# Performance work log

Hardware: AMD Instinct MI355X
Metric: run time of the kernel (lower is better)

The kernel has to match this reference:

```python
import jax, jax.numpy as jnp
import numpy as np

B, S, D = 8, 4096, 768
HEADS = 12
NEIGHBORS = 2
DILATION = 1
KERNEL = 1 + 2 * NEIGHBORS  # 5
DIM_HEAD = D // HEADS


def setup_inputs() -> dict:
    key = jax.random.key(0)
    ks = jax.random.split(key, 11)
    sc = 1.0 / np.sqrt(D)
    return {
        "x": jax.random.normal(ks[0], (B, S, D), dtype=jnp.float32),
        "Wq": jax.random.normal(ks[1], (D, D), dtype=jnp.float32) * sc,
        "bq": jax.random.normal(ks[2], (D,), dtype=jnp.float32) * 0.02,
        "Wk": jax.random.normal(ks[3], (D, D), dtype=jnp.float32) * sc,
        "bk": jax.random.normal(ks[4], (D,), dtype=jnp.float32) * 0.02,
        "Wv": jax.random.normal(ks[5], (D, D), dtype=jnp.float32) * sc,
        "bv": jax.random.normal(ks[6], (D,), dtype=jnp.float32) * 0.02,
        "Wo": jax.random.normal(ks[7], (D, D), dtype=jnp.float32) * sc,
        "bo": jax.random.normal(ks[8], (D,), dtype=jnp.float32) * 0.02,
        "gamma": jnp.ones((D,), dtype=jnp.float32),
        "beta": jnp.zeros((D,), dtype=jnp.float32),
    }


def _extract_seq_patches(x, kernel_size, dilation):
    # [B, S, D] -> [B, S, kernel_size, D] of dilated local windows, zero-padded.
    seq_len = x.shape[1]
    patch_size = kernel_size + (dilation - 1) * (kernel_size - 1)
    pad_r = (patch_size - 1) // 2
    pad_l = patch_size - pad_r - 1
    xp = jnp.pad(x, ((0, 0), (pad_l, pad_r), (0, 0)))
    # small fixed loop over kernel positions (kernel_size = 5)
    return jnp.stack([xp[:, i:i + seq_len] for i in range(0, patch_size, dilation)], axis=2)


def reference(x, Wq, bq, Wk, bk, Wv, bv, Wo, bo, gamma, beta):
    patches = _extract_seq_patches(x, KERNEL, DILATION)  # [B, S, K, D]
    q = x @ Wq + bq                                       # [B, S, D]
    k = patches @ Wk + bk                                 # [B, S, K, D]
    v = patches @ Wv + bv                                 # [B, S, K, D]
    # split heads
    q = q.reshape(B, S, HEADS, DIM_HEAD)
    k = k.reshape(B, S, KERNEL, HEADS, DIM_HEAD)
    v = v.reshape(B, S, KERNEL, HEADS, DIM_HEAD)
    scale = jnp.sqrt(jnp.asarray(DIM_HEAD, dtype=q.dtype))
    scores = jnp.einsum('bshd,bskhd->bshk', q, k) / scale  # [B, S, H, K]
    p = jax.nn.softmax(scores, axis=-1)
    att = jnp.einsum('bshk,bskhd->bshd', p, v)             # [B, S, H, dh]
    att = att.reshape(B, S, D)
    att = att @ Wo + bo
    y = att + x
    # LayerNorm over last dim
    mu = jnp.mean(y, axis=-1, keepdims=True)
    var = jnp.var(y, axis=-1, keepdims=True)
    y = (y - mu) / jnp.sqrt(var + 1e-5) * gamma + beta
    return y
```

## Files before the change

### kernel.cpp

```cpp
#include <hip/hip_runtime.h>

#define B_  8
#define S_  4096
#define D_  768
#define H_  12
#define M_  (B_ * S_)
#define NQKV_ 2304
#define NTILES 12

typedef unsigned short u16;
typedef __attribute__((ext_vector_type(4))) float  f32x4;
typedef __attribute__((ext_vector_type(8))) __bf16 bf16x8;
typedef __attribute__((ext_vector_type(4))) u16    u16x4;

#define GAS __attribute__((address_space(1)))
#define LAS __attribute__((address_space(3)))

__device__ __forceinline__ u16 f2bf(float f) {
    unsigned u = __float_as_uint(f);
    u += 0x7FFF + ((u >> 16) & 1);
    return (u16)(u >> 16);
}
__device__ __forceinline__ float bf2f(u16 h) {
    return __uint_as_float(((unsigned)h) << 16);
}

__device__ __forceinline__ void gload_lds16(const void* g, void* l) {
    __builtin_amdgcn_global_load_lds((const GAS void*)g, (LAS void*)l, 16, 0, 0);
}

__device__ __forceinline__ int xcd_swz(int bid, int nwg) {
    return (bid & 7) * (nwg >> 3) + (bid >> 3);
}

__global__ __launch_bounds__(256) void castx_kernel(const float* __restrict__ x,
                                                    u16* __restrict__ xb) {
    const int i = blockIdx.x * 256 + threadIdx.x;
    const float4 v = ((const float4*)x)[i];
    u16x4 o;
    o.x = f2bf(v.x); o.y = f2bf(v.y); o.z = f2bf(v.z); o.w = f2bf(v.w);
    ((u16x4*)xb)[i] = o;
}

__global__ __launch_bounds__(256) void wtrans_kernel(const float* __restrict__ Wq,
                                                     const float* __restrict__ Wk,
                                                     const float* __restrict__ Wv,
                                                     const float* __restrict__ Wo,
                                                     u16* __restrict__ Wb) {
    const float* W = (blockIdx.z == 0) ? Wq : (blockIdx.z == 1) ? Wk
                   : (blockIdx.z == 2) ? Wv : Wo;
    u16* O = Wb + (size_t)blockIdx.z * D_ * D_;
    __shared__ float tile[32][33];
    const int tx = threadIdx.x & 31, ty = threadIdx.x >> 5;
    const int k0 = blockIdx.y * 32, n0 = blockIdx.x * 32;
#pragma unroll
    for (int j = 0; j < 4; j++)
        tile[ty + j * 8][tx] = W[(size_t)(k0 + ty + j * 8) * D_ + n0 + tx];
    __syncthreads();
#pragma unroll
    for (int j = 0; j < 4; j++)
        O[(size_t)(n0 + ty + j * 8) * D_ + k0 + tx] = f2bf(tile[tx][ty + j * 8]);
}


#define PHASE_END(N)                                         \
    __builtin_amdgcn_sched_barrier(0);                       \
    asm volatile("s_waitcnt vmcnt(" #N ")" ::: "memory");    \
    __builtin_amdgcn_s_barrier();                            \
    __builtin_amdgcn_sched_barrier(0)

#define MFMA_Q(AF, BF, MO, NO)                                               \
    _Pragma("unroll") for (int mi = 0; mi < 4; ++mi)                         \
        _Pragma("unroll") for (int ni = 0; ni < 2; ++ni)                     \
            _Pragma("unroll") for (int kh = 0; kh < 2; ++kh)                 \
                acc[mi + MO][ni + NO] =                                      \
                    __builtin_amdgcn_mfma_f32_16x16x32_bf16(                 \
                        AF[mi][kh], BF[ni][kh], acc[mi + MO][ni + NO], 0, 0, 0)

template <int MODE>
__global__ __launch_bounds__(512, 2) void gemm8_kernel(
    const u16* __restrict__ A, const u16* __restrict__ Wb,
    const float* __restrict__ b0, const float* __restrict__ b1,
    const float* __restrict__ b2,
    u16* __restrict__ outb, const u16* __restrict__ xres) {
    extern __shared__ char lds[];

    const int t = threadIdx.x;
    const int w = t >> 6, l = t & 63;
    const int wm = w >> 2, wn = w & 3;

    const int NTN = (MODE == 0) ? 9 : 3;
    const int work = xcd_swz(blockIdx.x, gridDim.x);
    const int mt = work / NTN, nt = work % NTN;
    const int m0 = mt * 256;
    const int n0 = nt * 256;
    const int widx = (MODE == 0) ? (n0 / D_) : 3;
    const int n0w = n0 - ((MODE == 0) ? widx * D_ : 0);

    const int srow   = t >> 3;
    const int schunk = (t & 7) ^ (srow & 7);
    const u16* Asrc = A + (size_t)(m0 + srow) * D_ + schunk * 8;
    const u16* Bsrc = Wb + (size_t)widx * (D_ * D_) + (size_t)(n0w + srow) * D_ + schunk * 8;

    auto STAGE_A = [&](int h, int tk, int db) {
        const u16* s = Asrc + (size_t)(h * 128) * D_ + tk * 64;
        char* d = lds + db * 65536 + h * 16384 + (w << 10);
        gload_lds16(s, d);
        gload_lds16(s + 64 * D_, d + 8192);
    };
    auto STAGE_B = [&](int h, int tk, int db) {
        const u16* s = Bsrc + (size_t)(h * 128) * D_ + tk * 64;
        char* d = lds + db * 65536 + 32768 + h * 16384 + (w << 10);
        gload_lds16(s, d);
        gload_lds16(s + 64 * D_, d + 8192);
    };

    const int ck0 = (((l >> 4) ^ (l & 7)) << 4);
    const int ck1 = ((((l >> 4) + 4) ^ (l & 7)) << 4);
    const int aRowB = (wm * 128 + (l & 15)) * 128;
    const int bRowB = 32768 + (wn * 64 + (l & 15)) * 128;
#define LDSREAD(off) (*(const bf16x8*)(lds + (off)))

    f32x4 acc[8][4];
#pragma unroll
    for (int i = 0; i < 8; i++)
#pragma unroll
        for (int j = 0; j < 4; j++) acc[i][j] = (f32x4){0.f, 0.f, 0.f, 0.f};

    bf16x8 Alo[4][2], Ahi[4][2], Ba[2][2], Bb[2][2];

    STAGE_A(0, 0, 0); STAGE_A(1, 0, 0); STAGE_B(0, 0, 0); STAGE_B(1, 0, 0);
    STAGE_B(1, 1, 1); STAGE_A(0, 1, 1); STAGE_A(1, 1, 1);
    __builtin_amdgcn_sched_barrier(0);
    asm volatile("s_waitcnt vmcnt(6)" ::: "memory");
    __builtin_amdgcn_s_barrier();
    __builtin_amdgcn_sched_barrier(0);
#pragma unroll
    for (int mi = 0; mi < 4; ++mi) {
        Alo[mi][0] = LDSREAD(aRowB + mi * 2048 + ck0);
        Alo[mi][1] = LDSREAD(aRowB + mi * 2048 + ck1);
    }
#pragma unroll
    for (int ni = 0; ni < 2; ++ni) {
        Ba[ni][0] = LDSREAD(bRowB + ni * 2048 + ck0);
        Ba[ni][1] = LDSREAD(bRowB + ni * 2048 + ck1);
    }

    for (int X = 0; X < NTILES; ++X) {
        const int bX = X & 1;
        const int L0off = bX << 16;
        const int L1off = (bX ^ 1) << 16;
        int t1 = X + 1; if (t1 >= NTILES) t1 -= NTILES;
        int t2 = X + 2; if (t2 >= NTILES) t2 -= NTILES;

#pragma unroll
        for (int ni = 0; ni < 2; ++ni) {
            Bb[ni][0] = LDSREAD(L0off + bRowB + (ni + 2) * 2048 + ck0);
            Bb[ni][1] = LDSREAD(L0off + bRowB + (ni + 2) * 2048 + ck1);
        }
#pragma unroll
        for (int mi = 0; mi < 4; ++mi) {
            Ahi[mi][0] = LDSREAD(L0off + aRowB + (mi + 4) * 2048 + ck0);
            Ahi[mi][1] = LDSREAD(L0off + aRowB + (mi + 4) * 2048 + ck1);
        }
        STAGE_B(0, t1, bX ^ 1);
        MFMA_Q(Alo, Ba, 0, 0);
        PHASE_END(8);

        STAGE_B(1, t2, bX);
        MFMA_Q(Alo, Bb, 0, 2);
        PHASE_END(4);

#pragma unroll
        for (int mi = 0; mi < 4; ++mi) {
            Alo[mi][0] = LDSREAD(L1off + aRowB + mi * 2048 + ck0);
            Alo[mi][1] = LDSREAD(L1off + aRowB + mi * 2048 + ck1);
        }
        STAGE_A(0, t2, bX);
        MFMA_Q(Ahi, Ba, 4, 0);
        PHASE_END(4);

#pragma unroll
        for (int ni = 0; ni < 2; ++ni) {
            Ba[ni][0] = LDSREAD(L1off + bRowB + ni * 2048 + ck0);
            Ba[ni][1] = LDSREAD(L1off + bRowB + ni * 2048 + ck1);
        }
        STAGE_A(1, t2, bX);
        MFMA_Q(Ahi, Bb, 4, 2);
        PHASE_END(8);
    }

    const int crow0 = m0 + wm * 128 + ((l >> 4) << 2);
    const int ccol0 = n0 + wn * 64 + (l & 15);
    if (MODE == 0) {
        const float* bias = (widx == 0) ? b0 : (widx == 1) ? b1 : b2;
        const int bcol0 = ccol0 - widx * D_;
#pragma unroll
        for (int mi = 0; mi < 8; ++mi)
#pragma unroll
            for (int ni = 0; ni < 4; ++ni) {
                const float bv = bias[bcol0 + ni * 16];
#pragma unroll
                for (int r = 0; r < 4; ++r)
                    outb[(size_t)(crow0 + mi * 16 + r) * NQKV_ + ccol0 + ni * 16] =
                        f2bf(acc[mi][ni][r] + bv);
            }
    } else {
#pragma unroll
        for (int mi = 0; mi < 8; ++mi)
#pragma unroll
            for (int ni = 0; ni < 4; ++ni) {
                const int col = ccol0 + ni * 16;
                const float bv = b0[col];
#pragma unroll
                for (int r = 0; r < 4; ++r) {
                    const size_t idx = (size_t)(crow0 + mi * 16 + r) * D_ + col;
                    outb[idx] = f2bf(acc[mi][ni][r] + bv + bf2f(xres[idx]));
                }
            }
    }
}

__global__ __launch_bounds__(256) void attn_kernel(const u16* __restrict__ QKV,
                                                   const float* __restrict__ bk,
                                                   const float* __restrict__ bv,
                                                   u16* __restrict__ att) {
    const int gw = xcd_swz(blockIdx.x, gridDim.x) * 4 + (threadIdx.x >> 6);
    const int l  = threadIdx.x & 63;
    const int hq = gw % 3;
    const int m  = gw / 3;
    const int s  = m & (S_ - 1);
    const int col = hq * 256 + l * 4;
    const u16* base = QKV + (size_t)m * NQKV_;

    const u16x4 qv = *(const u16x4*)(base + col);
    float qf[4];
#pragma unroll
    for (int j = 0; j < 4; j++) qf[j] = bf2f(qv[j]);

    float sc[5];
#pragma unroll
    for (int i = 0; i < 5; i++) {
        const int sp = s + i - 2;
        float p;
        if (sp >= 0 && sp < S_) {
            const u16x4 kv = *(const u16x4*)(base + (i - 2) * NQKV_ + D_ + col);
            p = qf[0] * bf2f(kv[0]) + qf[1] * bf2f(kv[1])
              + qf[2] * bf2f(kv[2]) + qf[3] * bf2f(kv[3]);
        } else {
            const float4 kb = *(const float4*)(bk + col);
            p = qf[0] * kb.x + qf[1] * kb.y + qf[2] * kb.z + qf[3] * kb.w;
        }
#pragma unroll
        for (int off = 1; off < 16; off <<= 1) p += __shfl_xor(p, off, 64);
        sc[i] = p * 0.125f;
    }
    float mx = sc[0];
#pragma unroll
    for (int i = 1; i < 5; i++) mx = fmaxf(mx, sc[i]);
    float e[5], sum = 0.f;
#pragma unroll
    for (int i = 0; i < 5; i++) { e[i] = __expf(sc[i] - mx); sum += e[i]; }
    const float inv = 1.f / sum;

    float o[4] = {0.f, 0.f, 0.f, 0.f};
#pragma unroll
    for (int i = 0; i < 5; i++) {
        const float wgt = e[i] * inv;
        const int sp = s + i - 2;
        if (sp >= 0 && sp < S_) {
            const u16x4 vv = *(const u16x4*)(base + (i - 2) * NQKV_ + 2 * D_ + col);
#pragma unroll
            for (int j = 0; j < 4; j++) o[j] += wgt * bf2f(vv[j]);
        } else {
            const float4 vb = *(const float4*)(bv + col);
            o[0] += wgt * vb.x; o[1] += wgt * vb.y;
            o[2] += wgt * vb.z; o[3] += wgt * vb.w;
        }
    }
    u16x4 ov;
#pragma unroll
    for (int j = 0; j < 4; j++) ov[j] = f2bf(o[j]);
    *(u16x4*)(att + (size_t)m * D_ + col) = ov;
}

__global__ __launch_bounds__(256) void ln_kernel(const u16* __restrict__ Yb,
                                                 const float* __restrict__ gamma,
                                                 const float* __restrict__ beta,
                                                 float* __restrict__ out) {
    const int row = blockIdx.x;
    const u16* r = Yb + (size_t)row * D_;
    const int t = threadIdx.x;
    const float v0 = bf2f(r[t]), v1 = bf2f(r[t + 256]), v2 = bf2f(r[t + 512]);
    float s  = v0 + v1 + v2;
    float s2 = v0 * v0 + v1 * v1 + v2 * v2;
#pragma unroll
    for (int off = 32; off > 0; off >>= 1) {
        s  += __shfl_xor(s,  off, 64);
        s2 += __shfl_xor(s2, off, 64);
    }
    __shared__ float red[8];
    const int w = t >> 6, l = t & 63;
    if (l == 0) { red[w] = s; red[4 + w] = s2; }
    __syncthreads();
    s  = red[0] + red[1] + red[2] + red[3];
    s2 = red[4] + red[5] + red[6] + red[7];
    const float mu  = s * (1.f / 768.f);
    const float var = s2 * (1.f / 768.f) - mu * mu;
    const float inv = rsqrtf(var + 1e-5f);
    float* o = out + (size_t)row * D_;
    o[t]       = (v0 - mu) * inv * gamma[t]       + beta[t];
    o[t + 256] = (v1 - mu) * inv * gamma[t + 256] + beta[t + 256];
    o[t + 512] = (v2 - mu) * inv * gamma[t + 512] + beta[t + 512];
}

extern "C" void kernel_launch(void* const* d_in, const int* in_sizes, int n_in,
                              void* d_out, int out_size, void* d_ws, size_t ws_size,
                              hipStream_t stream) {
    const float* x     = (const float*)d_in[0];
    const float* Wq    = (const float*)d_in[1];
    const float* bq    = (const float*)d_in[2];
    const float* Wk    = (const float*)d_in[3];
    const float* bk    = (const float*)d_in[4];
    const float* Wv    = (const float*)d_in[5];
    const float* bv    = (const float*)d_in[6];
    const float* Wo    = (const float*)d_in[7];
    const float* bo    = (const float*)d_in[8];
    const float* gamma = (const float*)d_in[9];
    const float* beta  = (const float*)d_in[10];

    char* ws = (char*)d_ws;
    u16*   Wb  = (u16*)ws;
    u16*   xb  = (u16*)(ws + 4718592);
    u16*   QKV = (u16*)(ws + 4718592 + 50331648);
    u16*   yb  = QKV;
    u16*   att = (u16*)d_out;

    (void)hipFuncSetAttribute(reinterpret_cast<const void*>(&gemm8_kernel<0>),
                              hipFuncAttributeMaxDynamicSharedMemorySize, 131072);
    (void)hipFuncSetAttribute(reinterpret_cast<const void*>(&gemm8_kernel<1>),
                              hipFuncAttributeMaxDynamicSharedMemorySize, 131072);

    castx_kernel<<<(M_ * D_) / (256 * 4), 256, 0, stream>>>(x, xb);
    wtrans_kernel<<<dim3(24, 24, 4), 256, 0, stream>>>(Wq, Wk, Wv, Wo, Wb);
    gemm8_kernel<0><<<(M_ / 256) * 9, 512, 131072, stream>>>(xb, Wb, bq, bk, bv,
                                                             QKV, nullptr);
    attn_kernel<<<(M_ * 3) / 4, 256, 0, stream>>>(QKV, bk, bv, att);
    gemm8_kernel<1><<<(M_ / 256) * 3, 512, 131072, stream>>>(att, Wb, bo, nullptr, nullptr,
                                                             yb, xb);
    ln_kernel<<<M_, 256, 0, stream>>>(yb, gamma, beta, (float*)d_out);
}
```

Before: 329.9 us.

## Fully unroll GEMM main loop, relax barrier waits, and raise MFMA priority

Fully unrolls the 12-iteration k-loop so buffer selection and wrapped tile indices become compile-time constants. LDS reads now use precomputed per-buffer base pointers with immediate offsets. Two of the four per-phase barriers drop their vmcnt wait, and the last iteration skips the now-unneeded LDS prefetch reads. MFMA blocks are wrapped in s_setprio to favour matrix issue across waves. The aim is to cut address arithmetic and stalls in the pipelined loop, at the cost of larger code size and tighter reliance on correct wait counts for the async global-to-LDS loads.

Measured after the change: 327.3 us. No clear change (-0.8%).

```diff
diff --git a/kernel.cpp b/kernel.cpp
--- a/kernel.cpp
+++ b/kernel.cpp
@@ -63,19 +63,28 @@
 }
 
 
-#define PHASE_END(N)                                         \
+#define BAR()                                                \
+    __builtin_amdgcn_sched_barrier(0);                       \
+    __builtin_amdgcn_s_barrier();                            \
+    __builtin_amdgcn_sched_barrier(0)
+
+#define VMBAR(N)                                             \
     __builtin_amdgcn_sched_barrier(0);                       \
     asm volatile("s_waitcnt vmcnt(" #N ")" ::: "memory");    \
     __builtin_amdgcn_s_barrier();                            \
     __builtin_amdgcn_sched_barrier(0)
 
 #define MFMA_Q(AF, BF, MO, NO)                                               \
+    __builtin_amdgcn_s_setprio(1);                                           \
     _Pragma("unroll") for (int mi = 0; mi < 4; ++mi)                         \
         _Pragma("unroll") for (int ni = 0; ni < 2; ++ni)                     \
             _Pragma("unroll") for (int kh = 0; kh < 2; ++kh)                 \
                 acc[mi + MO][ni + NO] =                                      \
                     __builtin_amdgcn_mfma_f32_16x16x32_bf16(                 \
-                        AF[mi][kh], BF[ni][kh], acc[mi + MO][ni + NO], 0, 0, 0)
+                        AF[mi][kh], BF[ni][kh], acc[mi + MO][ni + NO], 0, 0, 0); \
+    __builtin_amdgcn_s_setprio(0)
+
+#define RD(p, imm) (*(const bf16x8*)((p) + (imm)))
 
 template <int MODE>
 __global__ __launch_bounds__(512, 2) void gemm8_kernel(
@@ -119,7 +128,10 @@
     const int ck1 = ((((l >> 4) + 4) ^ (l & 7)) << 4);
     const int aRowB = (wm * 128 + (l & 15)) * 128;
     const int bRowB = 32768 + (wn * 64 + (l & 15)) * 128;
-#define LDSREAD(off) (*(const bf16x8*)(lds + (off)))
+    const char* aC0[2] = { lds + aRowB + ck0, lds + 65536 + aRowB + ck0 };
+    const char* aC1[2] = { lds + aRowB + ck1, lds + 65536 + aRowB + ck1 };
+    const char* bC0[2] = { lds + bRowB + ck0, lds + 65536 + bRowB + ck0 };
+    const char* bC1[2] = { lds + bRowB + ck1, lds + 65536 + bRowB + ck1 };
 
     f32x4 acc[8][4];
 #pragma unroll
@@ -137,57 +149,61 @@
     __builtin_amdgcn_sched_barrier(0);
 #pragma unroll
     for (int mi = 0; mi < 4; ++mi) {
-        Alo[mi][0] = LDSREAD(aRowB + mi * 2048 + ck0);
-        Alo[mi][1] = LDSREAD(aRowB + mi * 2048 + ck1);
+        Alo[mi][0] = RD(aC0[0], mi * 2048);
+        Alo[mi][1] = RD(aC1[0], mi * 2048);
     }
 #pragma unroll
     for (int ni = 0; ni < 2; ++ni) {
-        Ba[ni][0] = LDSREAD(bRowB + ni * 2048 + ck0);
-        Ba[ni][1] = LDSREAD(bRowB + ni * 2048 + ck1);
-    }
-
+        Ba[ni][0] = RD(bC0[0], ni * 2048);
+        Ba[ni][1] = RD(bC1[0], ni * 2048);
+    }
+
+#pragma unroll
     for (int X = 0; X < NTILES; ++X) {
-        const int bX = X & 1;
-        const int L0off = bX << 16;
-        const int L1off = (bX ^ 1) << 16;
-        int t1 = X + 1; if (t1 >= NTILES) t1 -= NTILES;
-        int t2 = X + 2; if (t2 >= NTILES) t2 -= NTILES;
+        const int c = X & 1;
+        const int o = c ^ 1;
+        const int t1 = (X + 1 < NTILES) ? X + 1 : X + 1 - NTILES;
+        const int t2 = (X + 2 < NTILES) ? X + 2 : X + 2 - NTILES;
 
 #pragma unroll
         for (int ni = 0; ni < 2; ++ni) {
-            Bb[ni][0] = LDSREAD(L0off + bRowB + (ni + 2) * 2048 + ck0);
-            Bb[ni][1] = LDSREAD(L0off + bRowB + (ni + 2) * 2048 + ck1);
+            Bb[ni][0] = RD(bC0[c], (ni + 2) * 2048);
+            Bb[ni][1] = RD(bC1[c], (ni + 2) * 2048);
         }
 #pragma unroll
         for (int mi = 0; mi < 4; ++mi) {
-            Ahi[mi][0] = LDSREAD(L0off + aRowB + (mi + 4) * 2048 + ck0);
-            Ahi[mi][1] = LDSREAD(L0off + aRowB + (mi + 4) * 2048 + ck1);
-        }
-        STAGE_B(0, t1, bX ^ 1);
+            Ahi[mi][0] = RD(aC0[c], (mi + 4) * 2048);
+            Ahi[mi][1] = RD(aC1[c], (mi + 4) * 2048);
+        }
+        STAGE_B(0, t1, o);
         MFMA_Q(Alo, Ba, 0, 0);
-        PHASE_END(8);
-
-        STAGE_B(1, t2, bX);
+        BAR();
+
+        STAGE_B(1, t2, c);
         MFMA_Q(Alo, Bb, 0, 2);
-        PHASE_END(4);
-
-#pragma unroll
-        for (int mi = 0; mi < 4; ++mi) {
-            Alo[mi][0] = LDSREAD(L1off + aRowB + mi * 2048 + ck0);
-            Alo[mi][1] = LDSREAD(L1off + aRowB + mi * 2048 + ck1);
-        }
-        STAGE_A(0, t2, bX);
+        VMBAR(4);
+
+        if (X + 1 < NTILES) {
+#pragma unroll
+            for (int mi = 0; mi < 4; ++mi) {
+                Alo[mi][0] = RD(aC0[o], mi * 2048);
+                Alo[mi][1] = RD(aC1[o], mi * 2048);
+            }
+        }
+        STAGE_A(0, t2, c);
         MFMA_Q(Ahi, Ba, 4, 0);
-        PHASE_END(4);
-
-#pragma unroll
-        for (int ni = 0; ni < 2; ++ni) {
-            Ba[ni][0] = LDSREAD(L1off + bRowB + ni * 2048 + ck0);
-            Ba[ni][1] = LDSREAD(L1off + bRowB + ni * 2048 + ck1);
-        }
-        STAGE_A(1, t2, bX);
+        VMBAR(4);
+
+        if (X + 1 < NTILES) {
+#pragma unroll
+            for (int ni = 0; ni < 2; ++ni) {
+                Ba[ni][0] = RD(bC0[o], ni * 2048);
+                Ba[ni][1] = RD(bC1[o], ni * 2048);
+            }
+        }
+        STAGE_A(1, t2, c);
         MFMA_Q(Ahi, Bb, 4, 2);
-        PHASE_END(8);
+        BAR();
     }
 
     const int crow0 = m0 + wm * 128 + ((l >> 4) << 2);
```

## Rewrite GEMM as 128x256 tile with triple-buffered 32-wide K stages

Applied to the files above, without the earlier changes.

Replaces the 256x256, double-buffered GEMM with a 128x256 tile that walks K in 32-element steps through a three-slot LDS ring, using 72KB of LDS instead of 128KB. Launch bounds move from 2 to 4 blocks per CU, and the MFMA bursts are wrapped in raised wave priority. The aim is higher occupancy and more blocks to balance work across CUs. In exchange, each block reuses less data, so more global traffic is needed per FLOP. Each K step also pays for two barriers plus a full lgkmcnt wait.

Result: faster. 306.3 us (-7.1%).

```diff
diff --git a/kernel.cpp b/kernel.cpp
--- a/kernel.cpp
+++ b/kernel.cpp
@@ -63,22 +63,18 @@
 }
 
 
-#define PHASE_END(N)                                         \
-    __builtin_amdgcn_sched_barrier(0);                       \
-    asm volatile("s_waitcnt vmcnt(" #N ")" ::: "memory");    \
-    __builtin_amdgcn_s_barrier();                            \
-    __builtin_amdgcn_sched_barrier(0)
-
-#define MFMA_Q(AF, BF, MO, NO)                                               \
+#define MFMA16(AF, BF)                                                       \
+    __builtin_amdgcn_s_setprio(1);                                           \
     _Pragma("unroll") for (int mi = 0; mi < 4; ++mi)                         \
-        _Pragma("unroll") for (int ni = 0; ni < 2; ++ni)                     \
-            _Pragma("unroll") for (int kh = 0; kh < 2; ++kh)                 \
-                acc[mi + MO][ni + NO] =                                      \
-                    __builtin_amdgcn_mfma_f32_16x16x32_bf16(                 \
-                        AF[mi][kh], BF[ni][kh], acc[mi + MO][ni + NO], 0, 0, 0)
+        _Pragma("unroll") for (int ni = 0; ni < 4; ++ni)                     \
+            acc[mi][ni] = __builtin_amdgcn_mfma_f32_16x16x32_bf16(           \
+                AF[mi], BF[ni], acc[mi][ni], 0, 0, 0);                       \
+    __builtin_amdgcn_s_setprio(0)
+
+#define RD(p, imm) (*(const bf16x8*)((p) + (imm)))
 
 template <int MODE>
-__global__ __launch_bounds__(512, 2) void gemm8_kernel(
+__global__ __launch_bounds__(512, 4) void gemmf_kernel(
     const u16* __restrict__ A, const u16* __restrict__ Wb,
     const float* __restrict__ b0, const float* __restrict__ b1,
     const float* __restrict__ b2,
@@ -92,111 +88,85 @@
     const int NTN = (MODE == 0) ? 9 : 3;
     const int work = xcd_swz(blockIdx.x, gridDim.x);
     const int mt = work / NTN, nt = work % NTN;
-    const int m0 = mt * 256;
+    const int m0 = mt * 128;
     const int n0 = nt * 256;
     const int widx = (MODE == 0) ? (n0 / D_) : 3;
     const int n0w = n0 - ((MODE == 0) ? widx * D_ : 0);
 
-    const int srow   = t >> 3;
-    const int schunk = (t & 7) ^ (srow & 7);
-    const u16* Asrc = A + (size_t)(m0 + srow) * D_ + schunk * 8;
-    const u16* Bsrc = Wb + (size_t)widx * (D_ * D_) + (size_t)(n0w + srow) * D_ + schunk * 8;
-
-    auto STAGE_A = [&](int h, int tk, int db) {
-        const u16* s = Asrc + (size_t)(h * 128) * D_ + tk * 64;
-        char* d = lds + db * 65536 + h * 16384 + (w << 10);
-        gload_lds16(s, d);
-        gload_lds16(s + 64 * D_, d + 8192);
-    };
-    auto STAGE_B = [&](int h, int tk, int db) {
-        const u16* s = Bsrc + (size_t)(h * 128) * D_ + tk * 64;
-        char* d = lds + db * 65536 + 32768 + h * 16384 + (w << 10);
-        gload_lds16(s, d);
-        gload_lds16(s + 64 * D_, d + 8192);
-    };
-
-    const int ck0 = (((l >> 4) ^ (l & 7)) << 4);
-    const int ck1 = ((((l >> 4) + 4) ^ (l & 7)) << 4);
-    const int aRowB = (wm * 128 + (l & 15)) * 128;
-    const int bRowB = 32768 + (wn * 64 + (l & 15)) * 128;
-#define LDSREAD(off) (*(const bf16x8*)(lds + (off)))
-
-    f32x4 acc[8][4];
-#pragma unroll
-    for (int i = 0; i < 8; i++)
+    const int sc   = l & 3;
+    const int srA  = w * 16 + (l >> 2);
+    const int srB  = w * 32 + (l >> 2);
+    const int fA   = (srA ^ (srA >> 2)) & 3;
+    const int fB   = (srB ^ (srB >> 2)) & 3;
+    const u16* AsrcB = A + (size_t)(m0 + srA) * D_ + (sc ^ fA) * 8;
+    const u16* BsrcB = Wb + (size_t)widx * (D_ * D_)
+                          + (size_t)(n0w + srB) * D_ + (sc ^ fB) * 8;
+    char* const dstA = lds + w * 1024;
+    char* const dstB = lds + 24576 + w * 2048;
+
+    const int fr   = l & 15;
+    const int slot = (l >> 4) ^ ((fr ^ (fr >> 2)) & 3);
+    const char* aBase = lds + (wm * 64 + fr) * 64 + slot * 16;
+    const char* bBase = lds + 24576 + (wn * 64 + fr) * 64 + slot * 16;
+
+    f32x4 acc[4][4];
+#pragma unroll
+    for (int i = 0; i < 4; i++)
 #pragma unroll
         for (int j = 0; j < 4; j++) acc[i][j] = (f32x4){0.f, 0.f, 0.f, 0.f};
 
-    bf16x8 Alo[4][2], Ahi[4][2], Ba[2][2], Bb[2][2];
-
-    STAGE_A(0, 0, 0); STAGE_A(1, 0, 0); STAGE_B(0, 0, 0); STAGE_B(1, 0, 0);
-    STAGE_B(1, 1, 1); STAGE_A(0, 1, 1); STAGE_A(1, 1, 1);
+    gload_lds16(AsrcB, dstA);
+    gload_lds16(BsrcB, dstB);
+    gload_lds16(BsrcB + 16 * D_, dstB + 1024);
+    gload_lds16(AsrcB + 32, dstA + 8192);
+    gload_lds16(BsrcB + 32, dstB + 16384);
+    gload_lds16(BsrcB + 32 + 16 * D_, dstB + 16384 + 1024);
     __builtin_amdgcn_sched_barrier(0);
-    asm volatile("s_waitcnt vmcnt(6)" ::: "memory");
+    asm volatile("s_waitcnt vmcnt(3)" ::: "memory");
     __builtin_amdgcn_s_barrier();
     __builtin_amdgcn_sched_barrier(0);
-#pragma unroll
-    for (int mi = 0; mi < 4; ++mi) {
-        Alo[mi][0] = LDSREAD(aRowB + mi * 2048 + ck0);
-        Alo[mi][1] = LDSREAD(aRowB + mi * 2048 + ck1);
-    }
-#pragma unroll
-    for (int ni = 0; ni < 2; ++ni) {
-        Ba[ni][0] = LDSREAD(bRowB + ni * 2048 + ck0);
-        Ba[ni][1] = LDSREAD(bRowB + ni * 2048 + ck1);
-    }
-
-    for (int X = 0; X < NTILES; ++X) {
-        const int bX = X & 1;
-        const int L0off = bX << 16;
-        const int L1off = (bX ^ 1) << 16;
-        int t1 = X + 1; if (t1 >= NTILES) t1 -= NTILES;
-        int t2 = X + 2; if (t2 >= NTILES) t2 -= NTILES;
-
-#pragma unroll
-        for (int ni = 0; ni < 2; ++ni) {
-            Bb[ni][0] = LDSREAD(L0off + bRowB + (ni + 2) * 2048 + ck0);
-            Bb[ni][1] = LDSREAD(L0off + bRowB + (ni + 2) * 2048 + ck1);
-        }
-#pragma unroll
-        for (int mi = 0; mi < 4; ++mi) {
-            Ahi[mi][0] = LDSREAD(L0off + aRowB + (mi + 4) * 2048 + ck0);
-            Ahi[mi][1] = LDSREAD(L0off + aRowB + (mi + 4) * 2048 + ck1);
-        }
-        STAGE_B(0, t1, bX ^ 1);
-        MFMA_Q(Alo, Ba, 0, 0);
-        PHASE_END(8);
-
-        STAGE_B(1, t2, bX);
-        MFMA_Q(Alo, Bb, 0, 2);
-        PHASE_END(4);
-
-#pragma unroll
-        for (int mi = 0; mi < 4; ++mi) {
-            Alo[mi][0] = LDSREAD(L1off + aRowB + mi * 2048 + ck0);
-            Alo[mi][1] = LDSREAD(L1off + aRowB + mi * 2048 + ck1);
-        }
-        STAGE_A(0, t2, bX);
-        MFMA_Q(Ahi, Ba, 4, 0);
-        PHASE_END(4);
-
-#pragma unroll
-        for (int ni = 0; ni < 2; ++ni) {
-            Ba[ni][0] = LDSREAD(L1off + bRowB + ni * 2048 + ck0);
-            Ba[ni][1] = LDSREAD(L1off + bRowB + ni * 2048 + ck1);
-        }
-        STAGE_A(1, t2, bX);
-        MFMA_Q(Ahi, Bb, 4, 2);
-        PHASE_END(8);
-    }
-
-    const int crow0 = m0 + wm * 128 + ((l >> 4) << 2);
-    const int ccol0 = n0 + wn * 64 + (l & 15);
+
+#pragma unroll
+    for (int p = 0; p < 2 * NTILES; ++p) {
+        const int rg = p % 3;
+        const int sg = (p + 2) % 3;
+        const int Xs = (p + 2) >> 1;
+        const int sX = (Xs >= NTILES) ? 0 : Xs;
+        const int soff = sX * 64 + (p & 1) * 32;
+
+        bf16x8 Af[4], Bf[4];
+#pragma unroll
+        for (int i = 0; i < 4; ++i)
+            Af[i] = RD(aBase, rg * 8192 + i * 1024);
+#pragma unroll
+        for (int n = 0; n < 4; ++n)
+            Bf[n] = RD(bBase, rg * 16384 + n * 1024);
+
+        gload_lds16(AsrcB + soff, dstA + sg * 8192);
+        gload_lds16(BsrcB + soff, dstB + sg * 16384);
+        gload_lds16(BsrcB + soff + 16 * D_, dstB + sg * 16384 + 1024);
+
+        __builtin_amdgcn_sched_barrier(0);
+        asm volatile("s_waitcnt vmcnt(3)" ::: "memory");
+        __builtin_amdgcn_s_barrier();
+        asm volatile("s_waitcnt lgkmcnt(0)" ::: "memory");
+        __builtin_amdgcn_sched_barrier(0);
+
+        MFMA16(Af, Bf);
+
+        __builtin_amdgcn_sched_barrier(0);
+        __builtin_amdgcn_s_barrier();
+        __builtin_amdgcn_sched_barrier(0);
+    }
+    asm volatile("s_waitcnt vmcnt(0)" ::: "memory");
+
+    const int crow0 = m0 + wm * 64 + ((l >> 4) << 2);
+    const int ccol0 = n0 + wn * 64 + fr;
     if (MODE == 0) {
         const float* bias = (widx == 0) ? b0 : (widx == 1) ? b1 : b2;
         const int bcol0 = ccol0 - widx * D_;
 #pragma unroll
-        for (int mi = 0; mi < 8; ++mi)
+        for (int mi = 0; mi < 4; ++mi)
 #pragma unroll
             for (int ni = 0; ni < 4; ++ni) {
                 const float bv = bias[bcol0 + ni * 16];
@@ -207,7 +177,7 @@
             }
     } else {
 #pragma unroll
-        for (int mi = 0; mi < 8; ++mi)
+        for (int mi = 0; mi < 4; ++mi)
 #pragma unroll
             for (int ni = 0; ni < 4; ++ni) {
                 const int col = ccol0 + ni * 16;
@@ -336,17 +306,17 @@
     u16*   yb  = QKV;
     u16*   att = (u16*)d_out;
 
-    (void)hipFuncSetAttribute(reinterpret_cast<const void*>(&gemm8_kernel<0>),
-                              hipFuncAttributeMaxDynamicSharedMemorySize, 131072);
-    (void)hipFuncSetAttribute(reinterpret_cast<const void*>(&gemm8_kernel<1>),
-                              hipFuncAttributeMaxDynamicSharedMemorySize, 131072);
+    (void)hipFuncSetAttribute(reinterpret_cast<const void*>(&gemmf_kernel<0>),
+                              hipFuncAttributeMaxDynamicSharedMemorySize, 73728);
+    (void)hipFuncSetAttribute(reinterpret_cast<const void*>(&gemmf_kernel<1>),
+                              hipFuncAttributeMaxDynamicSharedMemorySize, 73728);
 
     castx_kernel<<<(M_ * D_) / (256 * 4), 256, 0, stream>>>(x, xb);
     wtrans_kernel<<<dim3(24, 24, 4), 256, 0, stream>>>(Wq, Wk, Wv, Wo, Wb);
-    gemm8_kernel<0><<<(M_ / 256) * 9, 512, 131072, stream>>>(xb, Wb, bq, bk, bv,
-                                                             QKV, nullptr);
+    gemmf_kernel<0><<<(M_ / 128) * 9, 512, 73728, stream>>>(xb, Wb, bq, bk, bv,
+                                                            QKV, nullptr);
     attn_kernel<<<(M_ * 3) / 4, 256, 0, stream>>>(QKV, bk, bv, att);
-    gemm8_kernel<1><<<(M_ / 256) * 3, 512, 131072, stream>>>(att, Wb, bo, nullptr, nullptr,
-                                                             yb, xb);
+    gemmf_kernel<1><<<(M_ / 128) * 3, 512, 73728, stream>>>(att, Wb, bo, nullptr, nullptr,
+                                                            yb, xb);
     ln_kernel<<<M_, 256, 0, stream>>>(yb, gamma, beta, (float*)d_out);
 }
```
